# Kernel tuning notes

Hardware: AMD Instinct MI355X
Metric: run time of the kernel (lower is better)

Reference implementation:

```python
import jax, jax.numpy as jnp
import numpy as np
from jax import lax

SOBEL_X = jnp.array([[-1., 0., 1.], [-2., 0., 2.], [-1., 0., 1.]], jnp.float32).reshape(1, 1, 3, 3)
SOBEL_Y = jnp.array([[1., 2., 1.], [0., 0., 0.], [-1., -2., -1.]], jnp.float32).reshape(1, 1, 3, 3)


def _edge_detect(img):
    dn = ('NCHW', 'OIHW', 'NCHW')
    ex = lax.conv_general_dilated(img, SOBEL_X, (1, 1), [(1, 1), (1, 1)], dimension_numbers=dn)
    ey = lax.conv_general_dilated(img, SOBEL_Y, (1, 1), [(1, 1), (1, 1)], dimension_numbers=dn)
    return jnp.abs(ex) + jnp.abs(ey)


def _point_sample(img, pts):
    # img [B,C,H,W], pts [B,N,2] in [0,1] (x=width first). Matches torch
    # F.grid_sample(img, 2*pts-1, bilinear, align_corners=False, zero padding).
    B, C, H, W = img.shape
    g = 2.0 * pts - 1.0
    gx = ((g[..., 0] + 1.0) * W - 1.0) * 0.5
    gy = ((g[..., 1] + 1.0) * H - 1.0) * 0.5
    x0 = jnp.floor(gx)
    y0 = jnp.floor(gy)
    wx1 = gx - x0
    wy1 = gy - y0
    flat = img.reshape(B, C, H * W)
    Np = pts.shape[1]

    def gather(xi, yi):
        valid = (xi >= 0) & (xi <= W - 1) & (yi >= 0) & (yi <= H - 1)
        xi_c = jnp.clip(xi, 0, W - 1).astype(jnp.int32)
        yi_c = jnp.clip(yi, 0, H - 1).astype(jnp.int32)
        lin = yi_c * W + xi_c  # [B,N]
        idx = jnp.broadcast_to(lin[:, None, :], (B, C, Np))
        return jnp.take_along_axis(flat, idx, axis=2) * valid[:, None, :]

    v = ((1 - wx1) * (1 - wy1))[:, None, :] * gather(x0, y0) \
        + (wx1 * (1 - wy1))[:, None, :] * gather(x0 + 1, y0) \
        + ((1 - wx1) * wy1)[:, None, :] * gather(x0, y0 + 1) \
        + (wx1 * wy1)[:, None, :] * gather(x0 + 1, y0 + 1)
    return v  # [B,C,N]


def _ln(x, g, b, eps=1e-5):
    m = jnp.mean(x, axis=-1, keepdims=True)
    v = jnp.mean((x - m) ** 2, axis=-1, keepdims=True)
    return (x - m) * lax.rsqrt(v + eps) * g + b


def _sampling_points(out, N, over_gen, rand_point, beta=0.75):
    # torch version is @torch.no_grad()
    out = lax.stop_gradient(out)
    B = out.shape[0]
    n_imp = int(beta * N)
    sorted_mask = -jnp.sort(-out, axis=1)  # sort channels descending
    og_map = _point_sample(sorted_mask, over_gen)  # [B,C,k*N]
    unc = -(og_map[:, 0] - og_map[:, 1])
    _, idx = lax.top_k(unc, n_imp)
    importance = jnp.take_along_axis(over_gen, idx[..., None], axis=1)  # [B,n_imp,2]
    edge_num = (N - n_imp) // 2
    crack = jax.nn.softmax(out, axis=1)[:, 1:2]
    edge = _edge_detect(crack)
    eh, ew = edge.shape[-2], edge.shape[-1]
    _, eidx = lax.top_k(edge.reshape(B, -1), edge_num)
    # Faithful to torch: float division results are copied back into a long
    # tensor, truncating toward zero (these coords collapse to 0 since idx < h*w).
    c0 = jnp.trunc(eidx.astype(jnp.float32) / ew / eh)
    c1 = jnp.trunc((eidx % ew).astype(jnp.float32) / ew)
    coverage = jnp.stack([c0, c1], axis=-1)
    return jnp.concatenate([importance, coverage, rand_point], axis=1)  # [B,N,2]


def setup_inputs() -> dict:
    key = jax.random.key(0)
    ks = jax.random.split(key, 12)
    B, in_c, C, Hx, Hf = 8, 512, 2, 1024, 128
    N = Hx // 8  # 128
    n_imp = int(0.75 * N)  # 96
    edge_num = (N - n_imp) // 2  # 16
    rand_num = N - n_imp - edge_num  # 16
    x = jax.random.normal(ks[0], (B, 3, Hx, Hx), jnp.float32)
    res2 = jax.random.normal(ks[1], (B, in_c, Hf, Hf), jnp.float32)
    out = jax.random.normal(ks[2], (B, C, Hf, Hf), jnp.float32)
    over_gen = jax.random.uniform(ks[3], (B, 3 * N, 2), jnp.float32)
    rand_point = jax.random.uniform(ks[4], (B, rand_num, 2), jnp.float32)
    dropout_mask = (jax.random.uniform(ks[5], (B, C, N)) > 0.2).astype(jnp.float32) / 0.8
    std = 0.02
    h2 = in_c // 2
    w1 = jax.random.normal(ks[6], (in_c + C, in_c), jnp.float32) * std
    w2 = jax.random.normal(ks[7], (in_c, h2), jnp.float32) * std
    w3 = jax.random.normal(ks[8], (h2, C), jnp.float32) * std
    return {"x": x, "res2": res2, "out": out, "over_gen": over_gen,
            "rand_point": rand_point, "dropout_mask": dropout_mask,
            "w1": w1, "b1": jnp.zeros(in_c), "g1": jnp.ones(in_c), "be1": jnp.zeros(in_c),
            "w2": w2, "b2": jnp.zeros(h2), "g2": jnp.ones(h2), "be2": jnp.zeros(h2),
            "w3": w3, "b3": jnp.zeros(C)}


def reference(x, res2, out, over_gen, rand_point, dropout_mask,
              w1, b1, g1, be1, w2, b2, g2, be2, w3, b3):
    N = x.shape[-1] // 8
    points = _sampling_points(out, N, over_gen, rand_point)  # [B,N,2]
    coarse = _point_sample(out, points)   # [B,C,N]
    fine = _point_sample(res2, points)    # [B,in_c,N]
    feat = jnp.concatenate([coarse, fine], axis=1).transpose(0, 2, 1)  # [B,N,in_c+C]
    h = jax.nn.gelu(_ln(feat @ w1 + b1, g1, be1), approximate=False)
    h = jax.nn.gelu(_ln(h @ w2 + b2, g2, be2), approximate=False)
    pred = (h @ w3 + b3).transpose(0, 2, 1)  # [B,C,N]
    rend = pred * dropout_mask + coarse  # Dropout(0.2) as explicit mask
    return rend, points
```

## Files before the change

kernel.cpp:

```cpp
#include <hip/hip_runtime.h>
#include <cstddef>

#pragma clang fp contract(off)

__device__ __forceinline__ float bf2f(unsigned short u) {
    unsigned int v = ((unsigned int)u) << 16;
    return __builtin_bit_cast(float, v);
}
__device__ __forceinline__ unsigned short f2bf(float f) {
    unsigned int x = __builtin_bit_cast(unsigned int, f);
    unsigned int r = (x + 0x7FFFu + ((x >> 16) & 1u)) >> 16;
    return (unsigned short)r;
}

template<bool BF16>
__device__ __forceinline__ float LD(const void* p, size_t i) {
    if constexpr (BF16) return bf2f(((const unsigned short*)p)[i]);
    else return ((const float*)p)[i];
}
template<bool BF16>
__device__ __forceinline__ void ST(void* p, size_t i, float v) {
    if constexpr (BF16) ((unsigned short*)p)[i] = f2bf(v);
    else ((float*)p)[i] = v;
}

__global__ void k_detect(const unsigned int* __restrict__ g1u, int* __restrict__ flag) {
    if (threadIdx.x == 0 && blockIdx.x == 0)
        *flag = (g1u[0] == 0x3F803F80u) ? 1 : 0;
}

struct Samp {
    int o00, o01, o10, o11;
    float w00, w01, w10, w11;
};
__device__ __forceinline__ float grid_coord(float p) {
    float g = 2.0f * p - 1.0f;
    return ((g + 1.0f) * 128.0f - 1.0f) * 0.5f;
}
__device__ __forceinline__ Samp mk_samp(float px, float py) {
    Samp s;
    float gx = grid_coord(px);
    float gy = grid_coord(py);
    float x0f = floorf(gx), y0f = floorf(gy);
    float wx1 = gx - x0f, wy1 = gy - y0f;
    float wx0 = 1.0f - wx1, wy0 = 1.0f - wy1;
    int x0 = (int)x0f, y0 = (int)y0f;
    int x1 = x0 + 1, y1 = y0 + 1;
    bool vx0 = (x0 >= 0) && (x0 < 128);
    bool vx1 = (x1 >= 0) && (x1 < 128);
    bool vy0 = (y0 >= 0) && (y0 < 128);
    bool vy1 = (y1 >= 0) && (y1 < 128);
    s.o00 = (vx0 && vy0) ? (y0 * 128 + x0) : -1;
    s.o01 = (vx1 && vy0) ? (y0 * 128 + x1) : -1;
    s.o10 = (vx0 && vy1) ? (y1 * 128 + x0) : -1;
    s.o11 = (vx1 && vy1) ? (y1 * 128 + x1) : -1;
    s.w00 = wx0 * wy0; s.w01 = wx1 * wy0;
    s.w10 = wx0 * wy1; s.w11 = wx1 * wy1;
    return s;
}
template<bool BF16>
__device__ __forceinline__ float samp_apply(const void* img, const Samp& s) {
    float v00 = (s.o00 >= 0) ? LD<BF16>(img, s.o00) : 0.f;
    float v01 = (s.o01 >= 0) ? LD<BF16>(img, s.o01) : 0.f;
    float v10 = (s.o10 >= 0) ? LD<BF16>(img, s.o10) : 0.f;
    float v11 = (s.o11 >= 0) ? LD<BF16>(img, s.o11) : 0.f;
    return ((s.w00 * v00 + s.w01 * v01) + s.w10 * v10) + s.w11 * v11;
}

template<bool BF16>
__global__ __launch_bounds__(384) void k_points(
    const void* __restrict__ out, const void* __restrict__ over_gen,
    const void* __restrict__ rand_point, const int* __restrict__ flag,
    void* __restrict__ d_out, float* __restrict__ pts_ws, float* __restrict__ coarse_ws)
{
    if ((*flag != 0) != BF16) return;
    int b = blockIdx.x;
    int tid = threadIdx.x;
    __shared__ float unc[384];
    __shared__ float pts[128][2];
    size_t outbase = (size_t)b * 2 * 16384;
    float px = LD<BF16>(over_gen, (size_t)(b * 384 + tid) * 2 + 0);
    float py = LD<BF16>(over_gen, (size_t)(b * 384 + tid) * 2 + 1);
    {
        Samp s = mk_samp(px, py);
        float M00 = 0.f, M01 = 0.f, M10 = 0.f, M11 = 0.f;
        float m00 = 0.f, m01 = 0.f, m10 = 0.f, m11 = 0.f;
        if (s.o00 >= 0) { float a = LD<BF16>(out, outbase + s.o00), c = LD<BF16>(out, outbase + 16384 + s.o00); M00 = fmaxf(a, c); m00 = fminf(a, c); }
        if (s.o01 >= 0) { float a = LD<BF16>(out, outbase + s.o01), c = LD<BF16>(out, outbase + 16384 + s.o01); M01 = fmaxf(a, c); m01 = fminf(a, c); }
        if (s.o10 >= 0) { float a = LD<BF16>(out, outbase + s.o10), c = LD<BF16>(out, outbase + 16384 + s.o10); M10 = fmaxf(a, c); m10 = fminf(a, c); }
        if (s.o11 >= 0) { float a = LD<BF16>(out, outbase + s.o11), c = LD<BF16>(out, outbase + 16384 + s.o11); M11 = fmaxf(a, c); m11 = fminf(a, c); }
        float og0 = ((s.w00 * M00 + s.w01 * M01) + s.w10 * M10) + s.w11 * M11;
        float og1 = ((s.w00 * m00 + s.w01 * m01) + s.w10 * m10) + s.w11 * m11;
        unc[tid] = og1 - og0;
    }
    __syncthreads();
    {
        float v = unc[tid];
        int rank = 0;
        for (int j = 0; j < 384; ++j) {
            float u = unc[j];
            rank += (u > v) || (u == v && j < tid);
        }
        if (rank < 96) { pts[rank][0] = px; pts[rank][1] = py; }
    }
    if (tid < 16) {
        pts[96 + tid][0] = 0.f; pts[96 + tid][1] = 0.f;
    } else if (tid < 32) {
        int r = tid - 16;
        pts[112 + r][0] = LD<BF16>(rand_point, (size_t)(b * 16 + r) * 2 + 0);
        pts[112 + r][1] = LD<BF16>(rand_point, (size_t)(b * 16 + r) * 2 + 1);
    }
    __syncthreads();
    if (tid < 128) {
        float qx = pts[tid][0], qy = pts[tid][1];
        pts_ws[(b * 128 + tid) * 2 + 0] = qx;
        pts_ws[(b * 128 + tid) * 2 + 1] = qy;
        ST<BF16>(d_out, 2048 + (size_t)(b * 128 + tid) * 2 + 0, qx);
        ST<BF16>(d_out, 2048 + (size_t)(b * 128 + tid) * 2 + 1, qy);
    }
    if (tid < 256) {
        int c = tid >> 7, n = tid & 127;
        Samp s = mk_samp(pts[n][0], pts[n][1]);
        coarse_ws[(b * 2 + c) * 128 + n] =
            samp_apply<BF16>((const void*)((const char*)out + ((size_t)(b * 2 + c) * 16384) * (BF16 ? 2 : 4)), s);
    }
}

template<bool BF16>
__global__ __launch_bounds__(512) void k_fine(
    const void* __restrict__ res2, const float* __restrict__ pts_ws,
    const float* __restrict__ coarse_ws, const int* __restrict__ flag,
    float* __restrict__ feat)
{
    if ((*flag != 0) != BF16) return;
    int blk = blockIdx.x;
    int b = blk >> 7, n = blk & 127;
    int ch = threadIdx.x;
    float px = pts_ws[blk * 2 + 0], py = pts_ws[blk * 2 + 1];
    Samp s = mk_samp(px, py);
    const void* img = (const void*)((const char*)res2 + ((size_t)(b * 512 + ch) * 16384) * (BF16 ? 2 : 4));
    feat[(size_t)blk * 514 + 2 + ch] = samp_apply<BF16>(img, s);
    if (ch < 2) feat[(size_t)blk * 514 + ch] = coarse_ws[(b * 2 + ch) * 128 + n];
}

template<bool BF16>
__global__ __launch_bounds__(256) void k_mlp1(
    const float* __restrict__ feat, const void* __restrict__ w1,
    const void* __restrict__ b1, const void* __restrict__ g1,
    const void* __restrict__ be1, const int* __restrict__ flag,
    float* __restrict__ h1)
{
    if ((*flag != 0) != BF16) return;
    __shared__ float lf[4 * 514];
    __shared__ float red_s[256];
    __shared__ float red_q[256];
    int blk = blockIdx.x;
    int b = blk >> 5, n0 = (blk & 31) * 4;
    int tid = threadIdx.x;
    const float* frow = feat + (size_t)(b * 128 + n0) * 514;
    for (int idx = tid; idx < 4 * 514; idx += 256) lf[idx] = frow[idx];
    __syncthreads();
    float acc[4][2];
#pragma unroll
    for (int r = 0; r < 4; ++r) { acc[r][0] = 0.f; acc[r][1] = 0.f; }
    for (int k = 0; k < 514; ++k) {
        float wa = LD<BF16>(w1, (size_t)k * 512 + tid);
        float wb = LD<BF16>(w1, (size_t)k * 512 + tid + 256);
#pragma unroll
        for (int r = 0; r < 4; ++r) {
            float f = lf[r * 514 + k];
            acc[r][0] = fmaf(f, wa, acc[r][0]);
            acc[r][1] = fmaf(f, wb, acc[r][1]);
        }
    }
    float bb0 = LD<BF16>(b1, tid), bb1 = LD<BF16>(b1, tid + 256);
    float ga = LD<BF16>(g1, tid), gb = LD<BF16>(g1, tid + 256);
    float ea = LD<BF16>(be1, tid), eb = LD<BF16>(be1, tid + 256);
    for (int r = 0; r < 4; ++r) {
        float v0 = acc[r][0] + bb0, v1 = acc[r][1] + bb1;
        red_s[tid] = v0 + v1;
        red_q[tid] = v0 * v0 + v1 * v1;
        __syncthreads();
        for (int s = 128; s > 0; s >>= 1) {
            if (tid < s) { red_s[tid] += red_s[tid + s]; red_q[tid] += red_q[tid + s]; }
            __syncthreads();
        }
        float m = red_s[0] * (1.f / 512.f);
        float var = red_q[0] * (1.f / 512.f) - m * m;
        float rstd = 1.f / sqrtf(var + 1e-5f);
        __syncthreads();
        float h0 = (v0 - m) * rstd * ga + ea;
        float h1v = (v1 - m) * rstd * gb + eb;
        h0  = 0.5f * h0  * (1.f + erff(h0  * 0.70710678118654752f));
        h1v = 0.5f * h1v * (1.f + erff(h1v * 0.70710678118654752f));
        h1[(size_t)(b * 128 + n0 + r) * 512 + tid]       = h0;
        h1[(size_t)(b * 128 + n0 + r) * 512 + tid + 256] = h1v;
    }
}

template<bool BF16>
__global__ __launch_bounds__(256) void k_mlp2(
    const float* __restrict__ h1, const void* __restrict__ w2,
    const void* __restrict__ b2, const void* __restrict__ g2,
    const void* __restrict__ be2, const int* __restrict__ flag,
    float* __restrict__ h2)
{
    if ((*flag != 0) != BF16) return;
    __shared__ float lf[4 * 512];
    __shared__ float red_s[256];
    __shared__ float red_q[256];
    int blk = blockIdx.x;
    int b = blk >> 5, n0 = (blk & 31) * 4;
    int tid = threadIdx.x;
    const float* frow = h1 + (size_t)(b * 128 + n0) * 512;
    for (int idx = tid; idx < 4 * 512; idx += 256) lf[idx] = frow[idx];
    __syncthreads();
    float acc[4] = {0.f, 0.f, 0.f, 0.f};
    for (int k = 0; k < 512; ++k) {
        float w = LD<BF16>(w2, (size_t)k * 256 + tid);
#pragma unroll
        for (int r = 0; r < 4; ++r) acc[r] = fmaf(lf[r * 512 + k], w, acc[r]);
    }
    float bb = LD<BF16>(b2, tid), ga = LD<BF16>(g2, tid), ea = LD<BF16>(be2, tid);
    for (int r = 0; r < 4; ++r) {
        float v = acc[r] + bb;
        red_s[tid] = v;
        red_q[tid] = v * v;
        __syncthreads();
        for (int s = 128; s > 0; s >>= 1) {
            if (tid < s) { red_s[tid] += red_s[tid + s]; red_q[tid] += red_q[tid + s]; }
            __syncthreads();
        }
        float m = red_s[0] * (1.f / 256.f);
        float var = red_q[0] * (1.f / 256.f) - m * m;
        float rstd = 1.f / sqrtf(var + 1e-5f);
        __syncthreads();
        float h = (v - m) * rstd * ga + ea;
        h = 0.5f * h * (1.f + erff(h * 0.70710678118654752f));
        h2[(size_t)(b * 128 + n0 + r) * 256 + tid] = h;
    }
}

template<bool BF16>
__global__ __launch_bounds__(256) void k_out(
    const float* __restrict__ h2, const void* __restrict__ w3,
    const void* __restrict__ b3, const void* __restrict__ mask,
    const float* __restrict__ coarse_ws, const int* __restrict__ flag,
    void* __restrict__ d_out)
{
    if ((*flag != 0) != BF16) return;
    int b = blockIdx.x, tid = threadIdx.x;
    int c = tid & 1, n = tid >> 1;
    const float* row = h2 + (size_t)(b * 128 + n) * 256;
    float acc = 0.f;
    for (int k = 0; k < 256; ++k) acc = fmaf(row[k], LD<BF16>(w3, (size_t)k * 2 + c), acc);
    float pred = acc + LD<BF16>(b3, c);
    int oi = b * 256 + c * 128 + n;
    float rend = pred * LD<BF16>(mask, oi) + coarse_ws[oi];
    ST<BF16>(d_out, oi, rend);
}

template<bool BF16>
static void launch_all(void* const* d_in, void* d_out, const int* flag,
                       float* pts_ws, float* coarse_ws, float* feat, float* h1, float* h2,
                       hipStream_t stream) {
    k_points<BF16><<<8, 384, 0, stream>>>(d_in[2], d_in[3], d_in[4], flag, d_out, pts_ws, coarse_ws);
    k_fine<BF16><<<8 * 128, 512, 0, stream>>>(d_in[1], pts_ws, coarse_ws, flag, feat);
    k_mlp1<BF16><<<8 * 32, 256, 0, stream>>>(feat, d_in[6], d_in[7], d_in[8], d_in[9], flag, h1);
    k_mlp2<BF16><<<8 * 32, 256, 0, stream>>>(h1, d_in[10], d_in[11], d_in[12], d_in[13], flag, h2);
    k_out<BF16><<<8, 256, 0, stream>>>(h2, d_in[14], d_in[15], d_in[5], coarse_ws, flag, d_out);
}

extern "C" void kernel_launch(void* const* d_in, const int* in_sizes, int n_in,
                              void* d_out, int out_size, void* d_ws, size_t ws_size,
                              hipStream_t stream) {
    int* flag = (int*)d_ws;
    float* fws = (float*)d_ws;
    float* pts_ws    = fws + 16;
    float* coarse_ws = pts_ws + 2048;
    float* feat      = coarse_ws + 2048;
    float* h1        = feat + 8 * 128 * 514;
    float* h2        = h1 + 8 * 128 * 512;

    k_detect<<<1, 1, 0, stream>>>((const unsigned int*)d_in[8], flag);
    launch_all<false>(d_in, d_out, flag, pts_ws, coarse_ws, feat, h1, h2, stream);
    launch_all<true>(d_in, d_out, flag, pts_ws, coarse_ws, feat, h1, h2, stream);
}
```

Baseline: 576.5 us.

## Fuse fine sampling and three-layer MLP into one kernel, drop dtype dispatch

Replaces the fine-sampling, two MLP layers and output kernels with a single fused kernel per 4-row tile. The feature vectors and hidden activations stay in shared memory, and the LayerNorm reductions use wave shuffles instead of a shared-memory tree. The runtime bf16/fp32 detection and the duplicate bf16 launch path are removed, so the code now assumes fp32 inputs. This cuts kernel launches and global round trips. In exchange it keeps only 256 blocks for the gather phase, which previously ran 1024 blocks, and it loses bf16 support.

```diff
diff --git a/kernel.cpp b/kernel.cpp
--- a/kernel.cpp
+++ b/kernel.cpp
@@ -2,32 +2,6 @@
 #include <cstddef>
 
 #pragma clang fp contract(off)
-
-__device__ __forceinline__ float bf2f(unsigned short u) {
-    unsigned int v = ((unsigned int)u) << 16;
-    return __builtin_bit_cast(float, v);
-}
-__device__ __forceinline__ unsigned short f2bf(float f) {
-    unsigned int x = __builtin_bit_cast(unsigned int, f);
-    unsigned int r = (x + 0x7FFFu + ((x >> 16) & 1u)) >> 16;
-    return (unsigned short)r;
-}
-
-template<bool BF16>
-__device__ __forceinline__ float LD(const void* p, size_t i) {
-    if constexpr (BF16) return bf2f(((const unsigned short*)p)[i]);
-    else return ((const float*)p)[i];
-}
-template<bool BF16>
-__device__ __forceinline__ void ST(void* p, size_t i, float v) {
-    if constexpr (BF16) ((unsigned short*)p)[i] = f2bf(v);
-    else ((float*)p)[i] = v;
-}
-
-__global__ void k_detect(const unsigned int* __restrict__ g1u, int* __restrict__ flag) {
-    if (threadIdx.x == 0 && blockIdx.x == 0)
-        *flag = (g1u[0] == 0x3F803F80u) ? 1 : 0;
-}
 
 struct Samp {
     int o00, o01, o10, o11;
@@ -58,37 +32,37 @@
     s.w10 = wx0 * wy1; s.w11 = wx1 * wy1;
     return s;
 }
-template<bool BF16>
-__device__ __forceinline__ float samp_apply(const void* img, const Samp& s) {
-    float v00 = (s.o00 >= 0) ? LD<BF16>(img, s.o00) : 0.f;
-    float v01 = (s.o01 >= 0) ? LD<BF16>(img, s.o01) : 0.f;
-    float v10 = (s.o10 >= 0) ? LD<BF16>(img, s.o10) : 0.f;
-    float v11 = (s.o11 >= 0) ? LD<BF16>(img, s.o11) : 0.f;
+__device__ __forceinline__ float samp_apply(const float* __restrict__ img, const Samp& s) {
+    float v00 = (s.o00 >= 0) ? img[s.o00] : 0.f;
+    float v01 = (s.o01 >= 0) ? img[s.o01] : 0.f;
+    float v10 = (s.o10 >= 0) ? img[s.o10] : 0.f;
+    float v11 = (s.o11 >= 0) ? img[s.o11] : 0.f;
     return ((s.w00 * v00 + s.w01 * v01) + s.w10 * v10) + s.w11 * v11;
 }
-
-template<bool BF16>
+__device__ __forceinline__ float gelu_exact(float h) {
+    return 0.5f * h * (1.f + erff(h * 0.70710678118654752f));
+}
+
 __global__ __launch_bounds__(384) void k_points(
-    const void* __restrict__ out, const void* __restrict__ over_gen,
-    const void* __restrict__ rand_point, const int* __restrict__ flag,
-    void* __restrict__ d_out, float* __restrict__ pts_ws, float* __restrict__ coarse_ws)
+    const float* __restrict__ out, const float* __restrict__ over_gen,
+    const float* __restrict__ rand_point,
+    float* __restrict__ d_out, float* __restrict__ pts_ws, float* __restrict__ coarse_ws)
 {
-    if ((*flag != 0) != BF16) return;
     int b = blockIdx.x;
     int tid = threadIdx.x;
     __shared__ float unc[384];
     __shared__ float pts[128][2];
     size_t outbase = (size_t)b * 2 * 16384;
-    float px = LD<BF16>(over_gen, (size_t)(b * 384 + tid) * 2 + 0);
-    float py = LD<BF16>(over_gen, (size_t)(b * 384 + tid) * 2 + 1);
+    float px = over_gen[(size_t)(b * 384 + tid) * 2 + 0];
+    float py = over_gen[(size_t)(b * 384 + tid) * 2 + 1];
     {
         Samp s = mk_samp(px, py);
         float M00 = 0.f, M01 = 0.f, M10 = 0.f, M11 = 0.f;
         float m00 = 0.f, m01 = 0.f, m10 = 0.f, m11 = 0.f;
-        if (s.o00 >= 0) { float a = LD<BF16>(out, outbase + s.o00), c = LD<BF16>(out, outbase + 16384 + s.o00); M00 = fmaxf(a, c); m00 = fminf(a, c); }
-        if (s.o01 >= 0) { float a = LD<BF16>(out, outbase + s.o01), c = LD<BF16>(out, outbase + 16384 + s.o01); M01 = fmaxf(a, c); m01 = fminf(a, c); }
-        if (s.o10 >= 0) { float a = LD<BF16>(out, outbase + s.o10), c = LD<BF16>(out, outbase + 16384 + s.o10); M10 = fmaxf(a, c); m10 = fminf(a, c); }
-        if (s.o11 >= 0) { float a = LD<BF16>(out, outbase + s.o11), c = LD<BF16>(out, outbase + 16384 + s.o11); M11 = fmaxf(a, c); m11 = fminf(a, c); }
+        if (s.o00 >= 0) { float a = out[outbase + s.o00], c = out[outbase + 16384 + s.o00]; M00 = fmaxf(a, c); m00 = fminf(a, c); }
+        if (s.o01 >= 0) { float a = out[outbase + s.o01], c = out[outbase + 16384 + s.o01]; M01 = fmaxf(a, c); m01 = fminf(a, c); }
+        if (s.o10 >= 0) { float a = out[outbase + s.o10], c = out[outbase + 16384 + s.o10]; M10 = fmaxf(a, c); m10 = fminf(a, c); }
+        if (s.o11 >= 0) { float a = out[outbase + s.o11], c = out[outbase + 16384 + s.o11]; M11 = fmaxf(a, c); m11 = fminf(a, c); }
         float og0 = ((s.w00 * M00 + s.w01 * M01) + s.w10 * M10) + s.w11 * M11;
         float og1 = ((s.w00 * m00 + s.w01 * m01) + s.w10 * m10) + s.w11 * m11;
         unc[tid] = og1 - og0;
@@ -107,182 +81,192 @@
         pts[96 + tid][0] = 0.f; pts[96 + tid][1] = 0.f;
     } else if (tid < 32) {
         int r = tid - 16;
-        pts[112 + r][0] = LD<BF16>(rand_point, (size_t)(b * 16 + r) * 2 + 0);
-        pts[112 + r][1] = LD<BF16>(rand_point, (size_t)(b * 16 + r) * 2 + 1);
+        pts[112 + r][0] = rand_point[(size_t)(b * 16 + r) * 2 + 0];
+        pts[112 + r][1] = rand_point[(size_t)(b * 16 + r) * 2 + 1];
     }
     __syncthreads();
     if (tid < 128) {
         float qx = pts[tid][0], qy = pts[tid][1];
         pts_ws[(b * 128 + tid) * 2 + 0] = qx;
         pts_ws[(b * 128 + tid) * 2 + 1] = qy;
-        ST<BF16>(d_out, 2048 + (size_t)(b * 128 + tid) * 2 + 0, qx);
-        ST<BF16>(d_out, 2048 + (size_t)(b * 128 + tid) * 2 + 1, qy);
+        d_out[2048 + (size_t)(b * 128 + tid) * 2 + 0] = qx;
+        d_out[2048 + (size_t)(b * 128 + tid) * 2 + 1] = qy;
     }
     if (tid < 256) {
         int c = tid >> 7, n = tid & 127;
         Samp s = mk_samp(pts[n][0], pts[n][1]);
-        coarse_ws[(b * 2 + c) * 128 + n] =
-            samp_apply<BF16>((const void*)((const char*)out + ((size_t)(b * 2 + c) * 16384) * (BF16 ? 2 : 4)), s);
-    }
-}
-
-template<bool BF16>
-__global__ __launch_bounds__(512) void k_fine(
-    const void* __restrict__ res2, const float* __restrict__ pts_ws,
-    const float* __restrict__ coarse_ws, const int* __restrict__ flag,
-    float* __restrict__ feat)
+        coarse_ws[(b * 2 + c) * 128 + n] = samp_apply(out + (size_t)(b * 2 + c) * 16384, s);
+    }
+}
+
+#define ROWS 4
+__global__ __launch_bounds__(512) void k_fused(
+    const float* __restrict__ res2, const float* __restrict__ pts_ws,
+    const float* __restrict__ coarse_ws,
+    const float* __restrict__ w1, const float* __restrict__ b1,
+    const float* __restrict__ g1, const float* __restrict__ be1,
+    const float* __restrict__ w2, const float* __restrict__ b2,
+    const float* __restrict__ g2, const float* __restrict__ be2,
+    const float* __restrict__ w3, const float* __restrict__ b3,
+    const float* __restrict__ mask, float* __restrict__ d_out)
 {
-    if ((*flag != 0) != BF16) return;
+    __shared__ float feat[ROWS][514];
+    __shared__ float h1s[ROWS][512];
+    __shared__ float h2s[ROWS][256];
+    __shared__ float part2[256][ROWS];
+    __shared__ float pd[8][32];
+    __shared__ float red_s[8][ROWS], red_q[8][ROWS];
+    __shared__ float stat_m[ROWS], stat_r[ROWS];
+    __shared__ float ptsl[ROWS][2];
+
     int blk = blockIdx.x;
-    int b = blk >> 7, n = blk & 127;
-    int ch = threadIdx.x;
-    float px = pts_ws[blk * 2 + 0], py = pts_ws[blk * 2 + 1];
-    Samp s = mk_samp(px, py);
-    const void* img = (const void*)((const char*)res2 + ((size_t)(b * 512 + ch) * 16384) * (BF16 ? 2 : 4));
-    feat[(size_t)blk * 514 + 2 + ch] = samp_apply<BF16>(img, s);
-    if (ch < 2) feat[(size_t)blk * 514 + ch] = coarse_ws[(b * 2 + ch) * 128 + n];
-}
-
-template<bool BF16>
-__global__ __launch_bounds__(256) void k_mlp1(
-    const float* __restrict__ feat, const void* __restrict__ w1,
-    const void* __restrict__ b1, const void* __restrict__ g1,
-    const void* __restrict__ be1, const int* __restrict__ flag,
-    float* __restrict__ h1)
-{
-    if ((*flag != 0) != BF16) return;
-    __shared__ float lf[4 * 514];
-    __shared__ float red_s[256];
-    __shared__ float red_q[256];
-    int blk = blockIdx.x;
-    int b = blk >> 5, n0 = (blk & 31) * 4;
+    int b = blk >> 5, n0 = (blk & 31) * ROWS;
     int tid = threadIdx.x;
-    const float* frow = feat + (size_t)(b * 128 + n0) * 514;
-    for (int idx = tid; idx < 4 * 514; idx += 256) lf[idx] = frow[idx];
-    __syncthreads();
-    float acc[4][2];
-#pragma unroll
-    for (int r = 0; r < 4; ++r) { acc[r][0] = 0.f; acc[r][1] = 0.f; }
+    int wave = tid >> 6, lane = tid & 63;
+
+    if (tid < ROWS * 2)
+        ((float*)ptsl)[tid] = pts_ws[(size_t)(b * 128 + n0) * 2 + tid];
+    if (tid >= 64 && tid < 64 + ROWS * 2) {
+        int i = tid - 64, r = i >> 1, c = i & 1;
+        feat[r][c] = coarse_ws[(b * 2 + c) * 128 + (n0 + r)];
+    }
+    __syncthreads();
+
+#pragma unroll
+    for (int r = 0; r < ROWS; ++r) {
+        Samp s = mk_samp(ptsl[r][0], ptsl[r][1]);
+        const float* img = res2 + ((size_t)(b * 512 + tid) << 14);
+        feat[r][2 + tid] = samp_apply(img, s);
+    }
+    __syncthreads();
+
+    int col = tid;
+    float acc1[ROWS] = {0.f, 0.f, 0.f, 0.f};
     for (int k = 0; k < 514; ++k) {
-        float wa = LD<BF16>(w1, (size_t)k * 512 + tid);
-        float wb = LD<BF16>(w1, (size_t)k * 512 + tid + 256);
-#pragma unroll
-        for (int r = 0; r < 4; ++r) {
-            float f = lf[r * 514 + k];
-            acc[r][0] = fmaf(f, wa, acc[r][0]);
-            acc[r][1] = fmaf(f, wb, acc[r][1]);
-        }
-    }
-    float bb0 = LD<BF16>(b1, tid), bb1 = LD<BF16>(b1, tid + 256);
-    float ga = LD<BF16>(g1, tid), gb = LD<BF16>(g1, tid + 256);
-    float ea = LD<BF16>(be1, tid), eb = LD<BF16>(be1, tid + 256);
-    for (int r = 0; r < 4; ++r) {
-        float v0 = acc[r][0] + bb0, v1 = acc[r][1] + bb1;
-        red_s[tid] = v0 + v1;
-        red_q[tid] = v0 * v0 + v1 * v1;
+        float w = w1[(size_t)k * 512 + col];
+#pragma unroll
+        for (int r = 0; r < ROWS; ++r) acc1[r] = fmaf(feat[r][k], w, acc1[r]);
+    }
+    {
+        float bb = b1[col], ga = g1[col], ea = be1[col];
+        float v[ROWS];
+#pragma unroll
+        for (int r = 0; r < ROWS; ++r) v[r] = acc1[r] + bb;
+#pragma unroll
+        for (int r = 0; r < ROWS; ++r) {
+            float s = v[r], q = v[r] * v[r];
+            for (int off = 32; off > 0; off >>= 1) {
+                s += __shfl_down(s, off, 64);
+                q += __shfl_down(q, off, 64);
+            }
+            if (lane == 0) { red_s[wave][r] = s; red_q[wave][r] = q; }
+        }
         __syncthreads();
-        for (int s = 128; s > 0; s >>= 1) {
-            if (tid < s) { red_s[tid] += red_s[tid + s]; red_q[tid] += red_q[tid + s]; }
-            __syncthreads();
-        }
-        float m = red_s[0] * (1.f / 512.f);
-        float var = red_q[0] * (1.f / 512.f) - m * m;
-        float rstd = 1.f / sqrtf(var + 1e-5f);
+        if (tid < ROWS) {
+            float s = 0.f, q = 0.f;
+            for (int w8 = 0; w8 < 8; ++w8) { s += red_s[w8][tid]; q += red_q[w8][tid]; }
+            float m = s * (1.f / 512.f);
+            float var = q * (1.f / 512.f) - m * m;
+            stat_m[tid] = m;
+            stat_r[tid] = 1.f / sqrtf(var + 1e-5f);
+        }
         __syncthreads();
-        float h0 = (v0 - m) * rstd * ga + ea;
-        float h1v = (v1 - m) * rstd * gb + eb;
-        h0  = 0.5f * h0  * (1.f + erff(h0  * 0.70710678118654752f));
-        h1v = 0.5f * h1v * (1.f + erff(h1v * 0.70710678118654752f));
-        h1[(size_t)(b * 128 + n0 + r) * 512 + tid]       = h0;
-        h1[(size_t)(b * 128 + n0 + r) * 512 + tid + 256] = h1v;
-    }
-}
-
-template<bool BF16>
-__global__ __launch_bounds__(256) void k_mlp2(
-    const float* __restrict__ h1, const void* __restrict__ w2,
-    const void* __restrict__ b2, const void* __restrict__ g2,
-    const void* __restrict__ be2, const int* __restrict__ flag,
-    float* __restrict__ h2)
-{
-    if ((*flag != 0) != BF16) return;
-    __shared__ float lf[4 * 512];
-    __shared__ float red_s[256];
-    __shared__ float red_q[256];
-    int blk = blockIdx.x;
-    int b = blk >> 5, n0 = (blk & 31) * 4;
-    int tid = threadIdx.x;
-    const float* frow = h1 + (size_t)(b * 128 + n0) * 512;
-    for (int idx = tid; idx < 4 * 512; idx += 256) lf[idx] = frow[idx];
-    __syncthreads();
-    float acc[4] = {0.f, 0.f, 0.f, 0.f};
-    for (int k = 0; k < 512; ++k) {
-        float w = LD<BF16>(w2, (size_t)k * 256 + tid);
-#pragma unroll
-        for (int r = 0; r < 4; ++r) acc[r] = fmaf(lf[r * 512 + k], w, acc[r]);
-    }
-    float bb = LD<BF16>(b2, tid), ga = LD<BF16>(g2, tid), ea = LD<BF16>(be2, tid);
-    for (int r = 0; r < 4; ++r) {
-        float v = acc[r] + bb;
-        red_s[tid] = v;
-        red_q[tid] = v * v;
-        __syncthreads();
-        for (int s = 128; s > 0; s >>= 1) {
-            if (tid < s) { red_s[tid] += red_s[tid + s]; red_q[tid] += red_q[tid + s]; }
-            __syncthreads();
-        }
-        float m = red_s[0] * (1.f / 256.f);
-        float var = red_q[0] * (1.f / 256.f) - m * m;
-        float rstd = 1.f / sqrtf(var + 1e-5f);
-        __syncthreads();
-        float h = (v - m) * rstd * ga + ea;
-        h = 0.5f * h * (1.f + erff(h * 0.70710678118654752f));
-        h2[(size_t)(b * 128 + n0 + r) * 256 + tid] = h;
-    }
-}
-
-template<bool BF16>
-__global__ __launch_bounds__(256) void k_out(
-    const float* __restrict__ h2, const void* __restrict__ w3,
-    const void* __restrict__ b3, const void* __restrict__ mask,
-    const float* __restrict__ coarse_ws, const int* __restrict__ flag,
-    void* __restrict__ d_out)
-{
-    if ((*flag != 0) != BF16) return;
-    int b = blockIdx.x, tid = threadIdx.x;
-    int c = tid & 1, n = tid >> 1;
-    const float* row = h2 + (size_t)(b * 128 + n) * 256;
-    float acc = 0.f;
-    for (int k = 0; k < 256; ++k) acc = fmaf(row[k], LD<BF16>(w3, (size_t)k * 2 + c), acc);
-    float pred = acc + LD<BF16>(b3, c);
-    int oi = b * 256 + c * 128 + n;
-    float rend = pred * LD<BF16>(mask, oi) + coarse_ws[oi];
-    ST<BF16>(d_out, oi, rend);
-}
-
-template<bool BF16>
-static void launch_all(void* const* d_in, void* d_out, const int* flag,
-                       float* pts_ws, float* coarse_ws, float* feat, float* h1, float* h2,
-                       hipStream_t stream) {
-    k_points<BF16><<<8, 384, 0, stream>>>(d_in[2], d_in[3], d_in[4], flag, d_out, pts_ws, coarse_ws);
-    k_fine<BF16><<<8 * 128, 512, 0, stream>>>(d_in[1], pts_ws, coarse_ws, flag, feat);
-    k_mlp1<BF16><<<8 * 32, 256, 0, stream>>>(feat, d_in[6], d_in[7], d_in[8], d_in[9], flag, h1);
-    k_mlp2<BF16><<<8 * 32, 256, 0, stream>>>(h1, d_in[10], d_in[11], d_in[12], d_in[13], flag, h2);
-    k_out<BF16><<<8, 256, 0, stream>>>(h2, d_in[14], d_in[15], d_in[5], coarse_ws, flag, d_out);
+#pragma unroll
+        for (int r = 0; r < ROWS; ++r)
+            h1s[r][col] = gelu_exact((v[r] - stat_m[r]) * stat_r[r] * ga + ea);
+    }
+    __syncthreads();
+
+    int c2 = tid & 255, kh = tid >> 8;
+    float acc2[ROWS] = {0.f, 0.f, 0.f, 0.f};
+    for (int k = 0; k < 256; ++k) {
+        int kk = (kh << 8) + k;
+        float w = w2[(size_t)kk * 256 + c2];
+#pragma unroll
+        for (int r = 0; r < ROWS; ++r) acc2[r] = fmaf(h1s[r][kk], w, acc2[r]);
+    }
+    if (kh == 1) {
+#pragma unroll
+        for (int r = 0; r < ROWS; ++r) part2[c2][r] = acc2[r];
+    }
+    __syncthreads();
+    float v2[ROWS];
+    float ga2 = 0.f, ea2 = 0.f;
+    if (kh == 0) {
+        float bb2 = b2[c2];
+        ga2 = g2[c2]; ea2 = be2[c2];
+#pragma unroll
+        for (int r = 0; r < ROWS; ++r) {
+            v2[r] = (acc2[r] + part2[c2][r]) + bb2;
+            float s = v2[r], q = v2[r] * v2[r];
+            for (int off = 32; off > 0; off >>= 1) {
+                s += __shfl_down(s, off, 64);
+                q += __shfl_down(q, off, 64);
+            }
+            if (lane == 0) { red_s[wave][r] = s; red_q[wave][r] = q; }
+        }
+    }
+    __syncthreads();
+    if (tid < ROWS) {
+        float s = 0.f, q = 0.f;
+        for (int w4 = 0; w4 < 4; ++w4) { s += red_s[w4][tid]; q += red_q[w4][tid]; }
+        float m = s * (1.f / 256.f);
+        float var = q * (1.f / 256.f) - m * m;
+        stat_m[tid] = m;
+        stat_r[tid] = 1.f / sqrtf(var + 1e-5f);
+    }
+    __syncthreads();
+    if (kh == 0) {
+#pragma unroll
+        for (int r = 0; r < ROWS; ++r)
+            h2s[r][c2] = gelu_exact((v2[r] - stat_m[r]) * stat_r[r] * ga2 + ea2);
+    }
+    __syncthreads();
+
+    if (tid < 256) {
+        int rc = tid >> 5, l = tid & 31;
+        int r = rc >> 1, c = rc & 1;
+        float p = 0.f;
+        for (int k = l; k < 256; k += 32) p = fmaf(h2s[r][k], w3[k * 2 + c], p);
+        pd[rc][l] = p;
+    }
+    __syncthreads();
+    if (tid < 8) {
+        int r = tid >> 1, c = tid & 1;
+        float acc = 0.f;
+        for (int l = 0; l < 32; ++l) acc += pd[tid][l];
+        float pred = acc + b3[c];
+        int oi = b * 256 + c * 128 + (n0 + r);
+        d_out[oi] = pred * mask[oi] + coarse_ws[oi];
+    }
 }
 
 extern "C" void kernel_launch(void* const* d_in, const int* in_sizes, int n_in,
                               void* d_out, int out_size, void* d_ws, size_t ws_size,
                               hipStream_t stream) {
-    int* flag = (int*)d_ws;
+    const float* res2 = (const float*)d_in[1];
+    const float* out  = (const float*)d_in[2];
+    const float* over_gen   = (const float*)d_in[3];
+    const float* rand_point = (const float*)d_in[4];
+    const float* mask = (const float*)d_in[5];
+    const float* w1 = (const float*)d_in[6];
+    const float* b1 = (const float*)d_in[7];
+    const float* g1 = (const float*)d_in[8];
+    const float* be1 = (const float*)d_in[9];
+    const float* w2 = (const float*)d_in[10];
+    const float* b2 = (const float*)d_in[11];
+    const float* g2 = (const float*)d_in[12];
+    const float* be2 = (const float*)d_in[13];
+    const float* w3 = (const float*)d_in[14];
+    const float* b3 = (const float*)d_in[15];
+    float* o = (float*)d_out;
+
     float* fws = (float*)d_ws;
-    float* pts_ws    = fws + 16;
-    float* coarse_ws = pts_ws + 2048;
-    float* feat      = coarse_ws + 2048;
-    float* h1        = feat + 8 * 128 * 514;
-    float* h2        = h1 + 8 * 128 * 512;
-
-    k_detect<<<1, 1, 0, stream>>>((const unsigned int*)d_in[8], flag);
-    launch_all<false>(d_in, d_out, flag, pts_ws, coarse_ws, feat, h1, h2, stream);
-    launch_all<true>(d_in, d_out, flag, pts_ws, coarse_ws, feat, h1, h2, stream);
-}
+    float* pts_ws    = fws;
+    float* coarse_ws = fws + 2048;
+
+    k_points<<<8, 384, 0, stream>>>(out, over_gen, rand_point, o, pts_ws, coarse_ws);
+    k_fused<<<8 * 32, 512, 0, stream>>>(res2, pts_ws, coarse_ws,
+                                        w1, b1, g1, be1, w2, b2, g2, be2, w3, b3,
+                                        mask, o);
+}
```

New measurement: 510.1 us. 1.13x faster.
